# Kernel optimization log

Hardware: AMD Instinct MI355X
Metric: run time of the kernel (lower is better)

Reference implementation:

```python
import jax, jax.numpy as jnp
import numpy as np
import math

E = 1024
H = 16
R = 16
ALPHA = 16
SCALING = ALPHA / R
T, B, S = 2048, 2, 2048


def setup_inputs() -> dict:
    key = jax.random.key(0)
    ks = jax.random.split(key, 20)
    d = {
        "query": jax.random.normal(ks[0], (T, B, E), jnp.float32),
        "key": jax.random.normal(ks[1], (S, B, E), jnp.float32),
        "value": jax.random.normal(ks[2], (S, B, E), jnp.float32),
    }
    i = 3
    for name in ("q", "k", "v", "o"):
        d[name + "_w"] = jax.random.normal(ks[i], (E, E), jnp.float32) * 0.02; i += 1
        d[name + "_b"] = jax.random.normal(ks[i], (E,), jnp.float32) * 0.02; i += 1
        d[name + "_la"] = jax.random.normal(ks[i], (R, E), jnp.float32) * 0.02; i += 1
        d[name + "_lb"] = jax.random.normal(ks[i], (E, R), jnp.float32) * 0.02; i += 1
    return d


def _lora_linear(x, w, b, la, lb):
    # y = x @ w.T + b + scaling * (x @ la.T) @ lb.T
    return x @ w.T + b + SCALING * ((x @ la.T) @ lb.T)


def reference(query, key, value,
              q_w, q_b, q_la, q_lb,
              k_w, k_b, k_la, k_lb,
              v_w, v_b, v_la, v_lb,
              o_w, o_b, o_la, o_lb):
    tgt_len, bsz, embed_dim = query.shape
    src_len = key.shape[0]
    head_dim = embed_dim // H
    q = _lora_linear(query, q_w, q_b, q_la, q_lb)
    k = _lora_linear(key, k_w, k_b, k_la, k_lb)
    v = _lora_linear(value, v_w, v_b, v_la, v_lb)
    # (T, B, E) -> (B*H, T, hd)
    q = q.reshape(tgt_len, bsz * H, head_dim).transpose(1, 0, 2)
    k = k.reshape(src_len, bsz * H, head_dim).transpose(1, 0, 2)
    v = v.reshape(src_len, bsz * H, head_dim).transpose(1, 0, 2)
    scale = 1.0 / math.sqrt(float(head_dim))
    scores = jnp.einsum("btd,bsd->bts", q * scale, k)  # (B*H, T, S)
    attn = jax.nn.softmax(scores, axis=-1)
    out = jnp.einsum("bts,bsd->btd", attn, v)  # (B*H, T, hd)
    out = out.transpose(1, 0, 2).reshape(tgt_len * bsz, embed_dim)
    out = _lora_linear(out, o_w, o_b, o_la, o_lb)
    out = out.reshape(tgt_len, bsz, embed_dim)
    attn_w = attn.reshape(bsz, H, tgt_len, src_len).mean(axis=1)
    return out, attn_w
```

## Files before the change

kernel.cpp:

```cpp
#include <hip/hip_runtime.h>
#include <stdint.h>

#define E_DIM 1024
#define KAUG 1056
#define N_HEADS 16
#define HD 64
#define R_LORA 16
#define T_LEN 2048
#define B_SZ 2
#define S_LEN 2048
#define NROW 4096
#define Q_SCALE 0.1803368801111204f

#define XG_N ((size_t)NROW * KAUG)
#define WG_N ((size_t)E_DIM * KAUG)
#define HSZ  ((size_t)B_SZ * N_HEADS * T_LEN * HD)

typedef unsigned short USH;
typedef __bf16 bf16x8 __attribute__((ext_vector_type(8)));
typedef unsigned short ushort8 __attribute__((ext_vector_type(8)));
typedef float  f32x4  __attribute__((ext_vector_type(4)));
typedef float  f32x16 __attribute__((ext_vector_type(16)));
typedef unsigned int u32x2 __attribute__((ext_vector_type(2)));
typedef unsigned int u32x4 __attribute__((ext_vector_type(4)));

__device__ __forceinline__ USH f2bf(float f) {
    uint32_t u = __builtin_bit_cast(uint32_t, f);
    return (USH)((u + 0x7FFFu + ((u >> 16) & 1u)) >> 16);
}
__device__ __forceinline__ float bf2f(USH s) {
    uint32_t u = ((uint32_t)s) << 16;
    return __builtin_bit_cast(float, u);
}
__device__ __forceinline__ void async_cp16(const void* g, void* l) {
    __builtin_amdgcn_global_load_lds(
        (const __attribute__((address_space(1))) void*)g,
        (__attribute__((address_space(3))) void*)l, 16, 0, 0);
}
__device__ __forceinline__ uint32_t pack_bf_trunc(float x, float y) {
    return __builtin_amdgcn_perm(__builtin_bit_cast(uint32_t, y),
                                 __builtin_bit_cast(uint32_t, x), 0x07060302u);
}
__device__ __forceinline__ bf16x8 cvt8(float4 a, float4 b) {
    ushort8 u;
    u[0] = f2bf(a.x); u[1] = f2bf(a.y); u[2] = f2bf(a.z); u[3] = f2bf(a.w);
    u[4] = f2bf(b.x); u[5] = f2bf(b.y); u[6] = f2bf(b.z); u[7] = f2bf(b.w);
    return __builtin_bit_cast(bf16x8, u);
}

__global__ __launch_bounds__(256) void lora_aug_x3_kernel(
    const float* __restrict__ Xq, const float* __restrict__ Xk,
    const float* __restrict__ Xv,
    const float* __restrict__ laq, const float* __restrict__ lak,
    const float* __restrict__ lav, USH* __restrict__ Xg_base) {
    int n0 = blockIdx.x * 16, y = blockIdx.y, tid = threadIdx.x;
    const float* X  = (y == 0) ? Xq : (y == 1) ? Xk : Xv;
    const float* la = (y == 0) ? laq : (y == 1) ? lak : lav;
    USH* Xg = Xg_base + (size_t)y * XG_N;

    int w = tid >> 6, lane = tid & 63, quad = lane >> 4, l16 = lane & 15;

    const float* xrow = X + (size_t)(n0 + l16) * E_DIM;
    const float* lrow = la + (size_t)l16 * E_DIM;
    USH* grow = Xg + (size_t)(n0 + l16) * KAUG;

    const f32x4 fzero = {0.f, 0.f, 0.f, 0.f};
    f32x4 acc = fzero;

#pragma unroll
    for (int i = 0; i < 8; ++i) {
        int k = w * 256 + i * 32 + quad * 8;
        bf16x8 af = cvt8(*(const float4*)(xrow + k), *(const float4*)(xrow + k + 4));
        *(bf16x8*)(grow + k) = af;
        bf16x8 bf_ = cvt8(*(const float4*)(lrow + k), *(const float4*)(lrow + k + 4));
        acc = __builtin_amdgcn_mfma_f32_16x16x32_bf16(af, bf_, acc, 0, 0, 0);
    }

    __shared__ float red[4][16][17];
#pragma unroll
    for (int r = 0; r < 4; ++r) red[w][quad * 4 + r][l16] = acc[r];
    __syncthreads();

    int row = tid >> 4, col = tid & 15;
    float v = red[0][row][col] + red[1][row][col] + red[2][row][col] + red[3][row][col];
    USH* trow = Xg + (size_t)(n0 + row) * KAUG + 1024;
    trow[col] = f2bf(v);
    trow[16 + col] = (col == 0) ? f2bf(1.0f) : (USH)0;
}

__global__ __launch_bounds__(256) void lora_a_bf16_kernel(
    USH* __restrict__ Xg, const float* __restrict__ la) {
    int n0 = blockIdx.x * 16, tid = threadIdx.x;
    int w = tid >> 6, lane = tid & 63, quad = lane >> 4, l16 = lane & 15;

    const USH* grow = Xg + (size_t)(n0 + l16) * KAUG;
    const float* lrow = la + (size_t)l16 * E_DIM;

    const f32x4 fzero = {0.f, 0.f, 0.f, 0.f};
    f32x4 acc = fzero;

#pragma unroll
    for (int i = 0; i < 8; ++i) {
        int k = w * 256 + i * 32 + quad * 8;
        bf16x8 af = *(const bf16x8*)(grow + k);
        bf16x8 bf_ = cvt8(*(const float4*)(lrow + k), *(const float4*)(lrow + k + 4));
        acc = __builtin_amdgcn_mfma_f32_16x16x32_bf16(af, bf_, acc, 0, 0, 0);
    }

    __shared__ float red[4][16][17];
#pragma unroll
    for (int r = 0; r < 4; ++r) red[w][quad * 4 + r][l16] = acc[r];
    __syncthreads();

    int row = tid >> 4, col = tid & 15;
    float v = red[0][row][col] + red[1][row][col] + red[2][row][col] + red[3][row][col];
    USH* trow = Xg + (size_t)(n0 + row) * KAUG + 1024;
    trow[col] = f2bf(v);
    trow[16 + col] = (col == 0) ? f2bf(1.0f) : (USH)0;
}

__global__ __launch_bounds__(256) void aug_w4_kernel(
    const float* __restrict__ Wq, const float* __restrict__ lbq, const float* __restrict__ bq,
    const float* __restrict__ Wk, const float* __restrict__ lbk, const float* __restrict__ bk_,
    const float* __restrict__ Wv, const float* __restrict__ lbv, const float* __restrict__ bv_,
    const float* __restrict__ Wo, const float* __restrict__ lbo, const float* __restrict__ bo,
    USH* __restrict__ Wg_base) {
    int e = blockIdx.x, y = blockIdx.y, tid = threadIdx.x;
    const float* W    = (y == 0) ? Wq : (y == 1) ? Wk : (y == 2) ? Wv : Wo;
    const float* lb   = (y == 0) ? lbq : (y == 1) ? lbk : (y == 2) ? lbv : lbo;
    const float* bias = (y == 0) ? bq : (y == 1) ? bk_ : (y == 2) ? bv_ : bo;
    USH* Wg = Wg_base + (size_t)y * WG_N;

    float4 v = *(const float4*)(W + (size_t)e * E_DIM + tid * 4);
    ushort4 o;
    o.x = f2bf(v.x); o.y = f2bf(v.y); o.z = f2bf(v.z); o.w = f2bf(v.w);
    *(ushort4*)(Wg + (size_t)e * KAUG + tid * 4) = o;
    if (tid < 32) {
        float t = (tid < R_LORA) ? lb[(size_t)e * R_LORA + tid]
                                 : (tid == R_LORA ? bias[e] : 0.0f);
        Wg[(size_t)e * KAUG + 1024 + tid] = f2bf(t);
    }
}

__global__ __launch_bounds__(256) void gemm_qkv_kernel(
    const USH* __restrict__ Xg_base, const USH* __restrict__ Wg_base,
    USH* __restrict__ qkv_base) {
    __shared__ __align__(16) USH As[2][128 * 32];
    __shared__ __align__(16) USH Bs[2][128 * 32];

    int orig = blockIdx.x + (blockIdx.y << 3) + blockIdx.z * 256;
    int v_ = (orig & 7) * 96 + (orig >> 3);
    int e0 = (v_ & 7) * 128, n0 = ((v_ >> 3) & 31) * 128, z = v_ >> 8;

    const USH* Xg = Xg_base + (size_t)z * XG_N;
    const USH* Wg = Wg_base + (size_t)z * WG_N;
    USH* out = qkv_base + (size_t)z * HSZ;
    float scale = (z == 0) ? Q_SCALE : 1.0f;

    int tid = threadIdx.x;
    int wid = tid >> 6, lane = tid & 63, quad = lane >> 4, l16 = lane & 15;
    int wm = wid & 1, wn = wid >> 1;

    int r0 = wid * 16 + (lane >> 2);
    int k8 = (lane & 3) * 8;

    f32x4 acc[4][4];
    const f32x4 fzero = {0.f, 0.f, 0.f, 0.f};
#pragma unroll
    for (int i = 0; i < 4; ++i)
#pragma unroll
        for (int j = 0; j < 4; ++j) acc[i][j] = fzero;

    async_cp16(Xg + (size_t)(n0 + r0) * KAUG + k8,       As[0] + (wid * 16) * 32);
    async_cp16(Xg + (size_t)(n0 + 64 + r0) * KAUG + k8,  As[0] + (64 + wid * 16) * 32);
    async_cp16(Wg + (size_t)(e0 + r0) * KAUG + k8,       Bs[0] + (wid * 16) * 32);
    async_cp16(Wg + (size_t)(e0 + 64 + r0) * KAUG + k8,  Bs[0] + (64 + wid * 16) * 32);
    __syncthreads();

    int cur = 0;
    for (int kt = 0; kt < KAUG; kt += 32, cur ^= 1) {
        if (kt + 32 < KAUG) {
            int kn = kt + 32;
            async_cp16(Xg + (size_t)(n0 + r0) * KAUG + kn + k8,       As[cur ^ 1] + (wid * 16) * 32);
            async_cp16(Xg + (size_t)(n0 + 64 + r0) * KAUG + kn + k8,  As[cur ^ 1] + (64 + wid * 16) * 32);
            async_cp16(Wg + (size_t)(e0 + r0) * KAUG + kn + k8,       Bs[cur ^ 1] + (wid * 16) * 32);
            async_cp16(Wg + (size_t)(e0 + 64 + r0) * KAUG + kn + k8,  Bs[cur ^ 1] + (64 + wid * 16) * 32);
        }

        bf16x8 af[4], bfr[4];
#pragma unroll
        for (int i = 0; i < 4; ++i)
            af[i] = *(const bf16x8*)&As[cur][(wm * 64 + i * 16 + l16) * 32 + quad * 8];
#pragma unroll
        for (int j = 0; j < 4; ++j)
            bfr[j] = *(const bf16x8*)&Bs[cur][(wn * 64 + j * 16 + l16) * 32 + quad * 8];
#pragma unroll
        for (int i = 0; i < 4; ++i)
#pragma unroll
            for (int j = 0; j < 4; ++j)
                acc[i][j] = __builtin_amdgcn_mfma_f32_16x16x32_bf16(
                    af[i], bfr[j], acc[i][j], 0, 0, 0);

        __syncthreads();
    }

#pragma unroll
    for (int i = 0; i < 4; ++i) {
#pragma unroll
        for (int j = 0; j < 4; ++j) {
#pragma unroll
            for (int r = 0; r < 4; ++r) {
                int nr = n0 + wm * 64 + i * 16 + quad * 4 + r;
                int ec = e0 + wn * 64 + j * 16 + l16;
                float v = acc[i][j][r] * scale;
                int b = nr & 1, h = ec >> 6, d = ec & 63;
                if (z != 2) {
                    int t = nr >> 1;
                    out[(((size_t)(b * 16 + h) * T_LEN + t) << 6) + d] = f2bf(v);
                } else {
                    int s = nr >> 1;
                    out[(((size_t)(b * 16 + h) * HD + d) << 11) + s] = f2bf(v);
                }
            }
        }
    }
}

__global__ __launch_bounds__(256) void gemm_o_kernel(
    const USH* __restrict__ Xg, const USH* __restrict__ Wg,
    float* __restrict__ out) {
    __shared__ __align__(16) USH As[2][64 * 32];
    __shared__ __align__(16) USH Bs[2][128 * 32];

    int orig = blockIdx.x + (blockIdx.y << 3);
    int v_ = ((orig & 7) << 6) + (orig >> 3);
    int e0 = (v_ & 7) * 128, n0 = (v_ >> 3) * 64;

    int tid = threadIdx.x;
    int wid = tid >> 6, lane = tid & 63, quad = lane >> 4, l16 = lane & 15;
    int wm = wid & 1, wn = wid >> 1;
    int r0 = wid * 16 + (lane >> 2);
    int k8 = (lane & 3) * 8;

    f32x4 acc[2][4];
    const f32x4 fzero = {0.f, 0.f, 0.f, 0.f};
#pragma unroll
    for (int i = 0; i < 2; ++i)
#pragma unroll
        for (int j = 0; j < 4; ++j) acc[i][j] = fzero;

    async_cp16(Xg + (size_t)(n0 + r0) * KAUG + k8,       As[0] + (wid * 16) * 32);
    async_cp16(Wg + (size_t)(e0 + r0) * KAUG + k8,       Bs[0] + (wid * 16) * 32);
    async_cp16(Wg + (size_t)(e0 + 64 + r0) * KAUG + k8,  Bs[0] + (64 + wid * 16) * 32);
    __syncthreads();

    int cur = 0;
    for (int kt = 0; kt < KAUG; kt += 32, cur ^= 1) {
        if (kt + 32 < KAUG) {
            int kn = kt + 32;
            async_cp16(Xg + (size_t)(n0 + r0) * KAUG + kn + k8,       As[cur ^ 1] + (wid * 16) * 32);
            async_cp16(Wg + (size_t)(e0 + r0) * KAUG + kn + k8,       Bs[cur ^ 1] + (wid * 16) * 32);
            async_cp16(Wg + (size_t)(e0 + 64 + r0) * KAUG + kn + k8,  Bs[cur ^ 1] + (64 + wid * 16) * 32);
        }

        bf16x8 af[2], bfr[4];
#pragma unroll
        for (int i = 0; i < 2; ++i)
            af[i] = *(const bf16x8*)&As[cur][(wm * 32 + i * 16 + l16) * 32 + quad * 8];
#pragma unroll
        for (int j = 0; j < 4; ++j)
            bfr[j] = *(const bf16x8*)&Bs[cur][(wn * 64 + j * 16 + l16) * 32 + quad * 8];
#pragma unroll
        for (int i = 0; i < 2; ++i)
#pragma unroll
            for (int j = 0; j < 4; ++j)
                acc[i][j] = __builtin_amdgcn_mfma_f32_16x16x32_bf16(
                    af[i], bfr[j], acc[i][j], 0, 0, 0);

        __syncthreads();
    }

#pragma unroll
    for (int i = 0; i < 2; ++i)
#pragma unroll
        for (int j = 0; j < 4; ++j)
#pragma unroll
            for (int r = 0; r < 4; ++r) {
                int nr = n0 + wm * 32 + i * 16 + quad * 4 + r;
                int ec = e0 + wn * 64 + j * 16 + l16;
                out[(size_t)nr * E_DIM + ec] = acc[i][j][r];
            }
}

__global__ __launch_bounds__(256, 2) void flash_mfma_kernel(
    const USH* __restrict__ qp, const USH* __restrict__ kp,
    const USH* __restrict__ vpt, USH* __restrict__ ohg,
    float* __restrict__ lbuf) {
    __shared__ __align__(16) USH Ks[2][4096];
    __shared__ __align__(16) USH Vs[2][4096];

    int orig = blockIdx.x + (blockIdx.y << 4);
    int v_ = ((orig & 7) << 6) + (orig >> 3);
    int t0 = (v_ & 15) * 128, bh = v_ >> 4;

    int tid = threadIdx.x, w = tid >> 6, lane = tid & 63;
    int lo = lane & 31, hi = lane >> 5;
    size_t headO = (size_t)bh * (T_LEN * HD);
    int t_base = t0 + w * 32;

    bf16x8 bq[4];
    {
        const USH* qrow = qp + headO + (size_t)(t_base + lo) * HD + hi * 8;
#pragma unroll
        for (int kb = 0; kb < 4; ++kb)
            bq[kb] = *(const bf16x8*)(qrow + kb * 16);
    }

#pragma unroll
    for (int c = 0; c < 2; ++c) {
        int f = w * 2 + c;
        async_cp16(kp + headO + (size_t)((f >> 2) * 32 + lo) * HD + (f & 3) * 16 + hi * 8,
                   &Ks[0][f * 512]);
        async_cp16(vpt + headO + (size_t)((f >> 2) * 32 + lo) * S_LEN + (f & 3) * 16 + hi * 8,
                   &Vs[0][f * 512]);
    }
    __syncthreads();

    const f32x16 z16 = {0,0,0,0,0,0,0,0,0,0,0,0,0,0,0,0};
    f32x16 o0 = z16, o1 = z16;
    float lsum = 0.f;

    for (int it = 0; it < S_LEN / 64; ++it) {
        int cur = it & 1;
        if (it + 1 < S_LEN / 64) {
            int sn = (it + 1) * 64;
#pragma unroll
            for (int c = 0; c < 2; ++c) {
                int f = w * 2 + c;
                async_cp16(kp + headO + (size_t)(sn + (f >> 2) * 32 + lo) * HD + (f & 3) * 16 + hi * 8,
                           &Ks[cur ^ 1][f * 512]);
                async_cp16(vpt + headO + (size_t)((f >> 2) * 32 + lo) * S_LEN + sn + (f & 3) * 16 + hi * 8,
                           &Vs[cur ^ 1][f * 512]);
            }
        }

        f32x16 sc0 = z16, sc1 = z16;
        __builtin_amdgcn_s_setprio(1);
#pragma unroll
        for (int kb = 0; kb < 4; ++kb) {
            bf16x8 ak0 = *(const bf16x8*)&Ks[cur][(0 * 4 + kb) * 512 + lane * 8];
            sc0 = __builtin_amdgcn_mfma_f32_32x32x16_bf16(ak0, bq[kb], sc0, 0, 0, 0);
        }
#pragma unroll
        for (int kb = 0; kb < 4; ++kb) {
            bf16x8 ak1 = *(const bf16x8*)&Ks[cur][(1 * 4 + kb) * 512 + lane * 8];
            sc1 = __builtin_amdgcn_mfma_f32_32x32x16_bf16(ak1, bq[kb], sc1, 0, 0, 0);
        }
        __builtin_amdgcn_s_setprio(0);

        float ls0 = 0.f, ls1 = 0.f, ls2 = 0.f, ls3 = 0.f;
#pragma unroll
        for (int r = 0; r < 16; ++r) {
            float p0 = __builtin_amdgcn_exp2f(sc0[r]);
            float p1 = __builtin_amdgcn_exp2f(sc1[r]);
            sc0[r] = p0; sc1[r] = p1;
            if ((r & 3) == 0)      { ls0 += p0; ls0 += p1; }
            else if ((r & 3) == 1) { ls1 += p0; ls1 += p1; }
            else if ((r & 3) == 2) { ls2 += p0; ls2 += p1; }
            else                   { ls3 += p0; ls3 += p1; }
        }
        lsum += (ls0 + ls1) + (ls2 + ls3);

        bf16x8 pa[4];
#pragma unroll
        for (int st = 0; st < 2; ++st) {
#pragma unroll
            for (int hh = 0; hh < 2; ++hh) {
                const f32x16& s_ = st ? sc1 : sc0;
                uint32_t a0 = pack_bf_trunc(s_[hh * 8 + 0], s_[hh * 8 + 1]);
                uint32_t a1 = pack_bf_trunc(s_[hh * 8 + 2], s_[hh * 8 + 3]);
                uint32_t a2 = pack_bf_trunc(s_[hh * 8 + 4], s_[hh * 8 + 5]);
                uint32_t a3 = pack_bf_trunc(s_[hh * 8 + 6], s_[hh * 8 + 7]);
                u32x2 r02 = __builtin_amdgcn_permlane32_swap(a0, a2, false, false);
                u32x2 r13 = __builtin_amdgcn_permlane32_swap(a1, a3, false, false);
                u32x4 pd = {r02[0], r13[0], r02[1], r13[1]};
                pa[st * 2 + hh] = __builtin_bit_cast(bf16x8, pd);
            }
        }

        __builtin_amdgcn_s_setprio(1);
#pragma unroll
        for (int ks = 0; ks < 4; ++ks) {
            bf16x8 bv0 = *(const bf16x8*)&Vs[cur][(0 * 4 + ks) * 512 + lane * 8];
            o0 = __builtin_amdgcn_mfma_f32_32x32x16_bf16(pa[ks], bv0, o0, 0, 0, 0);
        }
#pragma unroll
        for (int ks = 0; ks < 4; ++ks) {
            bf16x8 bv1 = *(const bf16x8*)&Vs[cur][(1 * 4 + ks) * 512 + lane * 8];
            o1 = __builtin_amdgcn_mfma_f32_32x32x16_bf16(pa[ks], bv1, o1, 0, 0, 0);
        }
        __builtin_amdgcn_s_setprio(0);

        __syncthreads();
    }

    lsum += __shfl_xor(lsum, 32, 64);
    float rinv = 1.0f / lsum;

    int b = bh >> 4, h = bh & 15;
    float inv[16];
#pragma unroll
    for (int r = 0; r < 16; ++r) {
        int rr = (r & 3) + 8 * (r >> 2) + 4 * hi;
        inv[r] = __shfl(rinv, rr, 64);
    }
#pragma unroll
    for (int r = 0; r < 16; ++r) {
        int t = t_base + (r & 3) + 8 * (r >> 2) + 4 * hi;
        size_t nrow = (size_t)(t * 2 + b) * KAUG + h * 64;
        ohg[nrow + lo]      = f2bf(o0[r] * inv[r]);
        ohg[nrow + 32 + lo] = f2bf(o1[r] * inv[r]);
    }
    if (lane < 32)
        lbuf[(size_t)bh * T_LEN + t_base + lane] = rinv;
}

__global__ __launch_bounds__(256, 4) void attnw_mfma_kernel(
    const USH* __restrict__ qp, const USH* __restrict__ kp,
    const float* __restrict__ lbuf, float* __restrict__ aw) {
    __shared__ __align__(16) USH Ks[2][4096];

    int orig = blockIdx.x + (blockIdx.y << 5) + (blockIdx.z << 9);
    int v_ = ((orig & 7) << 7) + (orig >> 3);
    int s0 = (v_ & 31) * 64, t0 = ((v_ >> 5) & 15) * 128, b = v_ >> 9;

    int tid = threadIdx.x, w = tid >> 6, lane = tid & 63;
    int quad = lane >> 4, l16 = lane & 15;

    const f32x4 fzero = {0.f, 0.f, 0.f, 0.f};
    f32x4 acc[2][4];
#pragma unroll
    for (int i2 = 0; i2 < 2; ++i2)
#pragma unroll
        for (int j = 0; j < 4; ++j) acc[i2][j] = fzero;

    {
        size_t head0 = (size_t)(b * 16) * (T_LEN * HD);
#pragma unroll
        for (int half = 0; half < 2; ++half)
            async_cp16(kp + head0 + (size_t)(s0 + w * 16 + l16) * HD + half * 32 + quad * 8,
                       &Ks[0][w * 1024 + half * 512]);
    }
    __syncthreads();

    for (int h = 0; h < N_HEADS; ++h) {
        int bh = b * 16 + h;
        size_t head = (size_t)bh * (T_LEN * HD);
        int cur = h & 1;

        if (h + 1 < N_HEADS) {
            size_t headn = head + (size_t)(T_LEN * HD);
#pragma unroll
            for (int half = 0; half < 2; ++half)
                async_cp16(kp + headn + (size_t)(s0 + w * 16 + l16) * HD + half * 32 + quad * 8,
                           &Ks[cur ^ 1][w * 1024 + half * 512]);
        }

        bf16x8 aq[2][2];
#pragma unroll
        for (int i2 = 0; i2 < 2; ++i2) {
            int i = w * 2 + i2;
            const USH* qrow = qp + head + (size_t)(t0 + i * 16 + l16) * HD + quad * 8;
            aq[i2][0] = *(const bf16x8*)qrow;
            aq[i2][1] = *(const bf16x8*)(qrow + 32);
        }

        float il[2][4];
#pragma unroll
        for (int i2 = 0; i2 < 2; ++i2)
#pragma unroll
            for (int r = 0; r < 4; ++r) {
                int t = t0 + w * 32 + i2 * 16 + quad * 4 + r;
                il[i2][r] = lbuf[(size_t)bh * T_LEN + t];
            }

        bf16x8 bk[4][2];
#pragma unroll
        for (int j = 0; j < 4; ++j)
#pragma unroll
            for (int half = 0; half < 2; ++half)
                bk[j][half] = *(const bf16x8*)&Ks[cur][j * 1024 + half * 512 + quad * 128 + l16 * 8];

#pragma unroll
        for (int i2 = 0; i2 < 2; ++i2) {
#pragma unroll
            for (int j = 0; j < 4; ++j) {
                f32x4 s = __builtin_amdgcn_mfma_f32_16x16x32_bf16(aq[i2][0], bk[j][0], fzero, 0, 0, 0);
                s = __builtin_amdgcn_mfma_f32_16x16x32_bf16(aq[i2][1], bk[j][1], s, 0, 0, 0);
#pragma unroll
                for (int r = 0; r < 4; ++r)
                    acc[i2][j][r] += __builtin_amdgcn_exp2f(s[r]) * il[i2][r];
            }
        }

        __syncthreads();
    }

    const float inv_h = 1.0f / (float)N_HEADS;
#pragma unroll
    for (int i2 = 0; i2 < 2; ++i2)
#pragma unroll
        for (int j = 0; j < 4; ++j)
#pragma unroll
            for (int r = 0; r < 4; ++r) {
                int t = t0 + w * 32 + i2 * 16 + quad * 4 + r;
                aw[(size_t)b * T_LEN * S_LEN + (size_t)t * S_LEN + s0 + j * 16 + l16] =
                    acc[i2][j][r] * inv_h;
            }
}

extern "C" void kernel_launch(void* const* d_in, const int* in_sizes, int n_in,
                              void* d_out, int out_size, void* d_ws, size_t ws_size,
                              hipStream_t stream) {
    (void)in_sizes; (void)n_in; (void)out_size; (void)ws_size;

    const float* query = (const float*)d_in[0];
    const float* key_  = (const float*)d_in[1];
    const float* value = (const float*)d_in[2];
    const float* q_w = (const float*)d_in[3],  *q_b = (const float*)d_in[4];
    const float* q_la = (const float*)d_in[5], *q_lb = (const float*)d_in[6];
    const float* k_w = (const float*)d_in[7],  *k_b = (const float*)d_in[8];
    const float* k_la = (const float*)d_in[9], *k_lb = (const float*)d_in[10];
    const float* v_w = (const float*)d_in[11], *v_b = (const float*)d_in[12];
    const float* v_la = (const float*)d_in[13], *v_lb = (const float*)d_in[14];
    const float* o_w = (const float*)d_in[15], *o_b = (const float*)d_in[16];
    const float* o_la = (const float*)d_in[17], *o_lb = (const float*)d_in[18];

    USH* Xg   = (USH*)d_ws;
    USH* Wg   = Xg + 3 * XG_N;
    USH* qkv  = Wg + 4 * WG_N;
    USH* qp   = qkv;
    USH* kp   = qkv + HSZ;
    USH* vpt  = qkv + 2 * HSZ;
    float* lbuf = (float*)(qkv + 3 * HSZ);

    float* out = (float*)d_out;
    float* aw  = out + (size_t)T_LEN * B_SZ * E_DIM;

    dim3 blk(256);

    lora_aug_x3_kernel<<<dim3(NROW / 16, 3), blk, 0, stream>>>(
        query, key_, value, q_la, k_la, v_la, Xg);
    aug_w4_kernel<<<dim3(E_DIM, 4), blk, 0, stream>>>(
        q_w, q_lb, q_b, k_w, k_lb, k_b, v_w, v_lb, v_b, o_w, o_lb, o_b, Wg);
    gemm_qkv_kernel<<<dim3(E_DIM / 128, NROW / 128, 3), blk, 0, stream>>>(Xg, Wg, qkv);

    flash_mfma_kernel<<<dim3(T_LEN / 128, B_SZ * N_HEADS), blk, 0, stream>>>(
        qp, kp, vpt, Xg, lbuf);
    attnw_mfma_kernel<<<dim3(S_LEN / 64, T_LEN / 128, B_SZ), blk, 0, stream>>>(
        qp, kp, lbuf, aw);

    lora_a_bf16_kernel<<<NROW / 16, blk, 0, stream>>>(Xg, o_la);
    gemm_o_kernel<<<dim3(E_DIM / 128, NROW / 64), blk, 0, stream>>>(
        Xg, Wg + 3 * WG_N, out);
}
```

Baseline: 330.2 us.

## Software-pipeline PV MFMA one iteration behind QK to overlap exp with matrix work

Restructures the attention loop so that the P·V matrix multiply for iteration it-1 is issued right after the QK^T MFMAs of iteration it, and the final PV block runs after the loop. The V tile for the current step is loaded at the start of that iteration instead of one step ahead. This lets the exp/softmax VALU work overlap with the MFMA pipe. The trade-off is more live registers and a shorter prefetch lead for V, since V is now loaded only one iteration ahead of its use.

```diff
diff --git a/kernel.cpp b/kernel.cpp
--- a/kernel.cpp
+++ b/kernel.cpp
@@ -321,14 +321,13 @@
         int f = w * 2 + c;
         async_cp16(kp + headO + (size_t)((f >> 2) * 32 + lo) * HD + (f & 3) * 16 + hi * 8,
                    &Ks[0][f * 512]);
-        async_cp16(vpt + headO + (size_t)((f >> 2) * 32 + lo) * S_LEN + (f & 3) * 16 + hi * 8,
-                   &Vs[0][f * 512]);
     }
     __syncthreads();
 
     const f32x16 z16 = {0,0,0,0,0,0,0,0,0,0,0,0,0,0,0,0};
     f32x16 o0 = z16, o1 = z16;
     float lsum = 0.f;
+    bf16x8 pa_prev[4];
 
     for (int it = 0; it < S_LEN / 64; ++it) {
         int cur = it & 1;
@@ -339,8 +338,15 @@
                 int f = w * 2 + c;
                 async_cp16(kp + headO + (size_t)(sn + (f >> 2) * 32 + lo) * HD + (f & 3) * 16 + hi * 8,
                            &Ks[cur ^ 1][f * 512]);
-                async_cp16(vpt + headO + (size_t)((f >> 2) * 32 + lo) * S_LEN + sn + (f & 3) * 16 + hi * 8,
-                           &Vs[cur ^ 1][f * 512]);
+            }
+        }
+        {
+            int s0 = it * 64;
+#pragma unroll
+            for (int c = 0; c < 2; ++c) {
+                int f = w * 2 + c;
+                async_cp16(vpt + headO + (size_t)((f >> 2) * 32 + lo) * S_LEN + s0 + (f & 3) * 16 + hi * 8,
+                           &Vs[cur][f * 512]);
             }
         }
 
@@ -355,6 +361,19 @@
         for (int kb = 0; kb < 4; ++kb) {
             bf16x8 ak1 = *(const bf16x8*)&Ks[cur][(1 * 4 + kb) * 512 + lane * 8];
             sc1 = __builtin_amdgcn_mfma_f32_32x32x16_bf16(ak1, bq[kb], sc1, 0, 0, 0);
+        }
+
+        if (it > 0) {
+#pragma unroll
+            for (int ks = 0; ks < 4; ++ks) {
+                bf16x8 bv0 = *(const bf16x8*)&Vs[cur ^ 1][(0 * 4 + ks) * 512 + lane * 8];
+                o0 = __builtin_amdgcn_mfma_f32_32x32x16_bf16(pa_prev[ks], bv0, o0, 0, 0, 0);
+            }
+#pragma unroll
+            for (int ks = 0; ks < 4; ++ks) {
+                bf16x8 bv1 = *(const bf16x8*)&Vs[cur ^ 1][(1 * 4 + ks) * 512 + lane * 8];
+                o1 = __builtin_amdgcn_mfma_f32_32x32x16_bf16(pa_prev[ks], bv1, o1, 0, 0, 0);
+            }
         }
         __builtin_amdgcn_s_setprio(0);
 
@@ -371,7 +390,6 @@
         }
         lsum += (ls0 + ls1) + (ls2 + ls3);
 
-        bf16x8 pa[4];
 #pragma unroll
         for (int st = 0; st < 2; ++st) {
 #pragma unroll
@@ -384,24 +402,24 @@
                 u32x2 r02 = __builtin_amdgcn_permlane32_swap(a0, a2, false, false);
                 u32x2 r13 = __builtin_amdgcn_permlane32_swap(a1, a3, false, false);
                 u32x4 pd = {r02[0], r13[0], r02[1], r13[1]};
-                pa[st * 2 + hh] = __builtin_bit_cast(bf16x8, pd);
-            }
-        }
-
-        __builtin_amdgcn_s_setprio(1);
+                pa_prev[st * 2 + hh] = __builtin_bit_cast(bf16x8, pd);
+            }
+        }
+
+        __syncthreads();
+    }
+
+    {
 #pragma unroll
         for (int ks = 0; ks < 4; ++ks) {
-            bf16x8 bv0 = *(const bf16x8*)&Vs[cur][(0 * 4 + ks) * 512 + lane * 8];
-            o0 = __builtin_amdgcn_mfma_f32_32x32x16_bf16(pa[ks], bv0, o0, 0, 0, 0);
+            bf16x8 bv0 = *(const bf16x8*)&Vs[1][(0 * 4 + ks) * 512 + lane * 8];
+            o0 = __builtin_amdgcn_mfma_f32_32x32x16_bf16(pa_prev[ks], bv0, o0, 0, 0, 0);
         }
 #pragma unroll
         for (int ks = 0; ks < 4; ++ks) {
-            bf16x8 bv1 = *(const bf16x8*)&Vs[cur][(1 * 4 + ks) * 512 + lane * 8];
-            o1 = __builtin_amdgcn_mfma_f32_32x32x16_bf16(pa[ks], bv1, o1, 0, 0, 0);
-        }
-        __builtin_amdgcn_s_setprio(0);
-
-        __syncthreads();
+            bf16x8 bv1 = *(const bf16x8*)&Vs[1][(1 * 4 + ks) * 512 + lane * 8];
+            o1 = __builtin_amdgcn_mfma_f32_32x32x16_bf16(pa_prev[ks], bv1, o1, 0, 0, 0);
+        }
     }
 
     lsum += __shfl_xor(lsum, 32, 64);
```

Result: no change. 328.7 us (median of 2 runs) (-0.5%).
